# Optimization experiments

Measured on AMD Instinct MI355X. Metric: run time of the kernel, lower is better.

Reference implementation:

```python
import math
import jax, jax.numpy as jnp
import numpy as np

B, N, D, H = 8, 128, 256, 8
DK = D // H
SCALE = 0.02


def setup_inputs() -> dict:
    key = jax.random.key(0)
    ks = jax.random.split(key, 10)
    return {
        "query_node": jax.random.normal(ks[0], (B, N, D), jnp.float32),
        "value_node": jax.random.normal(ks[1], (B, N, D), jnp.float32),
        "key_edge": jax.random.normal(ks[2], (B, N, N, D), jnp.float32),
        "adj_matrix": jax.random.uniform(ks[3], (B, N, N), jnp.float32),  # pairwise distances >= 0
        "mask": jnp.ones((B, N), jnp.int32),
        "Wq": jax.random.normal(ks[4], (D, D), jnp.float32) * SCALE,
        "bq": jnp.zeros((D,), jnp.float32),
        "Wk": jax.random.normal(ks[5], (D, D), jnp.float32) * SCALE,
        "bk": jnp.zeros((D,), jnp.float32),
        "Wv": jax.random.normal(ks[6], (D, D), jnp.float32) * SCALE,
        "bv": jnp.zeros((D,), jnp.float32),
        "Wno": jax.random.normal(ks[7], (D, D), jnp.float32) * SCALE,
        "bno": jnp.zeros((D,), jnp.float32),
        "Weo": jax.random.normal(ks[8], (D, D), jnp.float32) * SCALE,
        "beo": jnp.zeros((D,), jnp.float32),
        "att_lambda": jnp.float32(0.1),
    }


def reference(query_node, value_node, key_edge, adj_matrix, mask,
              Wq, bq, Wk, bk, Wv, bv, Wno, bno, Weo, beo, att_lambda):
    # distance-kernelized adjacency: softmax(-lambda * dist) over neighbors
    adj = att_lambda * adj_matrix                                  # [B,N,N]
    adj = jnp.where(mask[:, None, :] == 0, jnp.inf, adj)
    adj = jax.nn.softmax(-adj, axis=-1)                            # [B,N,N]

    q = (query_node @ Wq.T + bq).reshape(B, N, H, DK).transpose(0, 2, 1, 3)      # [B,H,N,DK] bhmd
    k = (key_edge @ Wk.T + bk).reshape(B, N, N, H, DK).transpose(0, 3, 1, 2, 4)  # [B,H,N,N,DK] bhmnd
    v = (value_node @ Wv.T + bv).reshape(B, N, H, DK).transpose(0, 2, 1, 3)      # [B,H,N,DK] bhnd

    inv_sqrt = 1.0 / math.sqrt(DK)
    out_scores = jnp.einsum('bhmd,bhmnd->bhmn', q, k) * inv_sqrt
    in_scores = jnp.einsum('bhnd,bhmnd->bhnm', q, k) * inv_sqrt

    m4 = mask[:, None, None, :] == 0                               # [B,1,1,N]
    neg_inf = jnp.asarray(-jnp.inf, out_scores.dtype)
    out_scores = jnp.where(m4, neg_inf, out_scores)
    in_scores = jnp.where(m4, neg_inf, in_scores)

    out_attn = jax.nn.softmax(out_scores, axis=-1)
    in_attn = jax.nn.softmax(in_scores, axis=-1)

    # message = out_attn + in_attn - diag_embed(diag(out_attn))
    eye = jnp.eye(N, dtype=out_attn.dtype)
    message = out_attn + in_attn - out_attn * eye
    message = message * adj[:, None]                               # adjacency gating (dropout = identity at eval)

    node_hidden = jnp.einsum('bhmn,bhnd->bhmd', message, v)        # [B,H,N,DK]
    edge_hidden = message[..., None] * k                           # [B,H,N,N,DK] outer-product edge update

    node_hidden = node_hidden.transpose(0, 2, 1, 3).reshape(B, N, D)
    edge_hidden = edge_hidden.transpose(0, 2, 3, 1, 4).reshape(B, N, N, D)

    return (node_hidden @ Wno.T + bno, edge_hidden @ Weo.T + beo)
```

## Files before the change

kernel.cpp:

```cpp
#include <hip/hip_runtime.h>
#include <math.h>

#define Bc 8
#define Nc 128
#define Dc 256
#define Hc 8
#define DKc 32

typedef __attribute__((ext_vector_type(8))) short short8;
typedef __attribute__((ext_vector_type(4))) float floatx4;

__device__ __forceinline__ unsigned short f2bf(float f) {
  unsigned int u = __float_as_uint(f);
  u += 0x7FFFu + ((u >> 16) & 1u);
  return (unsigned short)(u >> 16);
}

__device__ __forceinline__ float bf2f(unsigned short s) {
  return __uint_as_float(((unsigned int)s) << 16);
}

__global__ __launch_bounds__(256) void cast_bf16_kernel(
    const float* __restrict__ src, unsigned short* __restrict__ dst, int n) {
  const int i = (blockIdx.x * 256 + threadIdx.x) * 4;
  if (i < n) {
    const float4 v = *(const float4*)&src[i];
    *(ushort4*)&dst[i] = make_ushort4(f2bf(v.x), f2bf(v.y), f2bf(v.z), f2bf(v.w));
  }
}

__global__ __launch_bounds__(256) void gemm_xwT_kernel(
    const float* __restrict__ X, const float* __restrict__ W,
    const float* __restrict__ bias, float* __restrict__ C, int M) {
  __shared__ float As[64][17];
  __shared__ float Ws[64][17];
  const int t = threadIdx.x;
  const int tx = t & 15;
  const int ty = t >> 4;
  const size_t row0 = (size_t)blockIdx.y * 64;
  const int col0 = blockIdx.x * 64;
  const int lr = t >> 2;
  const int lc = (t & 3) * 4;

  float acc[4][4] = {};

  for (int kk = 0; kk < 256; kk += 16) {
    float4 av = *(const float4*)&X[(row0 + lr) * 256 + kk + lc];
    float4 wv = *(const float4*)&W[(size_t)(col0 + lr) * 256 + kk + lc];
    As[lr][lc] = av.x; As[lr][lc + 1] = av.y; As[lr][lc + 2] = av.z; As[lr][lc + 3] = av.w;
    Ws[lr][lc] = wv.x; Ws[lr][lc + 1] = wv.y; Ws[lr][lc + 2] = wv.z; Ws[lr][lc + 3] = wv.w;
    __syncthreads();
#pragma unroll
    for (int e = 0; e < 16; ++e) {
      float a[4], w[4];
#pragma unroll
      for (int r = 0; r < 4; ++r) a[r] = As[ty * 4 + r][e];
#pragma unroll
      for (int c = 0; c < 4; ++c) w[c] = Ws[tx * 4 + c][e];
#pragma unroll
      for (int r = 0; r < 4; ++r)
#pragma unroll
        for (int c = 0; c < 4; ++c) acc[r][c] = fmaf(a[r], w[c], acc[r][c]);
    }
    __syncthreads();
  }

  const float4 bv = *(const float4*)&bias[col0 + tx * 4];
#pragma unroll
  for (int r = 0; r < 4; ++r) {
    float4 o;
    o.x = acc[r][0] + bv.x;
    o.y = acc[r][1] + bv.y;
    o.z = acc[r][2] + bv.z;
    o.w = acc[r][3] + bv.w;
    *(float4*)&C[(row0 + ty * 4 + r) * 256 + col0 + tx * 4] = o;
  }
}

__global__ __launch_bounds__(128) void adj_softmax_kernel(
    const float* __restrict__ adj, const int* __restrict__ mask,
    const float* __restrict__ lam_p, float* __restrict__ adjs) {
  __shared__ float red[128];
  const int bi = blockIdx.x;
  const int b = bi >> 7;
  const int j = threadIdx.x;
  const float lam = lam_p[0];
  float x = (mask[b * 128 + j] != 0) ? (-lam * adj[(size_t)bi * 128 + j]) : -INFINITY;
  red[j] = x; __syncthreads();
  for (int s = 64; s > 0; s >>= 1) { if (j < s) red[j] = fmaxf(red[j], red[j + s]); __syncthreads(); }
  const float mx = red[0]; __syncthreads();
  const float e = expf(x - mx);
  red[j] = e; __syncthreads();
  for (int s = 64; s > 0; s >>= 1) { if (j < s) red[j] += red[j + s]; __syncthreads(); }
  const float z = red[0];
  adjs[(size_t)bi * 128 + j] = e / z;
}

__global__ __launch_bounds__(256) void kscore_kernel(
    const float* __restrict__ ke, const float* __restrict__ q,
    const unsigned short* __restrict__ wk, const float* __restrict__ bk,
    float* __restrict__ osc, float* __restrict__ isc,
    float* __restrict__ edge ) {
  __shared__ __align__(16) unsigned short As[64 * 40];
  __shared__ __align__(16) unsigned short Ws[256 * 40];
  const int nblk = blockIdx.x;
  const int bm = blockIdx.y;
  const int b = bm >> 7;
  const int m = bm & 127;
  const int n0 = nblk * 64;
  const int t = threadIdx.x;
  const int l = t & 63;
  const int w = t >> 6;
  const int lr = l & 15;
  const int lk = l >> 4;
  const size_t rowbase = ((size_t)bm * 128 + n0) * 256;
  unsigned short* kbf = (unsigned short*)edge;

  floatx4 acc[4][4] = {};

  for (int kk = 0; kk < 256; kk += 32) {
    float4 av[2]; int arow[2], akc[2];
#pragma unroll
    for (int p = 0; p < 2; ++p) {
      const int f = p * 256 + t;
      arow[p] = f >> 3; akc[p] = (f & 7) * 4;
      av[p] = *(const float4*)&ke[rowbase + (size_t)arow[p] * 256 + kk + akc[p]];
    }
    uint4 wv[4];
#pragma unroll
    for (int p = 0; p < 4; ++p) {
      const int f = p * 256 + t;
      const int row = f >> 2, kc = (f & 3) * 8;
      wv[p] = *(const uint4*)&wk[(size_t)row * 256 + kk + kc];
    }
    __syncthreads();
#pragma unroll
    for (int p = 0; p < 2; ++p)
      *(ushort4*)&As[arow[p] * 40 + akc[p]] =
          make_ushort4(f2bf(av[p].x), f2bf(av[p].y), f2bf(av[p].z), f2bf(av[p].w));
#pragma unroll
    for (int p = 0; p < 4; ++p) {
      const int f = p * 256 + t;
      const int row = f >> 2, kc = (f & 3) * 8;
      *(uint4*)&Ws[row * 40 + kc] = wv[p];
    }
    __syncthreads();
    short8 a[4], bw[4];
#pragma unroll
    for (int i = 0; i < 4; ++i)
      a[i] = *(const short8*)&As[(i * 16 + lr) * 40 + lk * 8];
#pragma unroll
    for (int j = 0; j < 4; ++j)
      bw[j] = *(const short8*)&Ws[(w * 64 + j * 16 + lr) * 40 + lk * 8];
#pragma unroll
    for (int i = 0; i < 4; ++i)
#pragma unroll
      for (int j = 0; j < 4; ++j)
        acc[i][j] = __builtin_amdgcn_mfma_f32_16x16x32_bf16(bw[j], a[i], acc[i][j], 0, 0, 0);
  }

  const float inv_sqrt = 0.17677669529663687f;
  float4 qm4[4], kb4[4];
#pragma unroll
  for (int j = 0; j < 4; ++j) {
    qm4[j] = *(const float4*)&q[((size_t)(b * 128 + m)) * 256 + w * 64 + j * 16 + lk * 4];
    kb4[j] = *(const float4*)&bk[w * 64 + j * 16 + lk * 4];
  }
#pragma unroll
  for (int i = 0; i < 4; ++i) {
    const int ng = n0 + i * 16 + lr;
    const size_t gkb = (size_t)bm * 128 + ng;
    const size_t qnb = ((size_t)(b * 128 + ng)) * 256 + w * 64 + lk * 4;
    float po0 = 0.f, po1 = 0.f, pi0 = 0.f, pi1 = 0.f;
#pragma unroll
    for (int j = 0; j < 4; ++j) {
      const float4 qn = *(const float4*)&q[qnb + j * 16];
      const float k0 = acc[i][j][0] + kb4[j].x;
      const float k1 = acc[i][j][1] + kb4[j].y;
      const float k2 = acc[i][j][2] + kb4[j].z;
      const float k3 = acc[i][j][3] + kb4[j].w;
      *(ushort4*)&kbf[gkb * 512 + 256 + w * 64 + j * 16 + lk * 4] =
          make_ushort4(f2bf(k0), f2bf(k1), f2bf(k2), f2bf(k3));
      const float so = fmaf(k0, qm4[j].x, fmaf(k1, qm4[j].y, fmaf(k2, qm4[j].z, k3 * qm4[j].w)));
      const float si = fmaf(k0, qn.x, fmaf(k1, qn.y, fmaf(k2, qn.z, k3 * qn.w)));
      if (j < 2) { po0 += so; pi0 += si; } else { po1 += so; pi1 += si; }
    }
    po0 += __shfl_xor(po0, 16, 64); po0 += __shfl_xor(po0, 32, 64);
    po1 += __shfl_xor(po1, 16, 64); po1 += __shfl_xor(po1, 32, 64);
    pi0 += __shfl_xor(pi0, 16, 64); pi0 += __shfl_xor(pi0, 32, 64);
    pi1 += __shfl_xor(pi1, 16, 64); pi1 += __shfl_xor(pi1, 32, 64);
    if (lk == 0) {
      const int h0 = w * 2, h1 = w * 2 + 1;
      osc[((size_t)(b * 8 + h0) * 128 + m) * 128 + ng] = po0 * inv_sqrt;
      osc[((size_t)(b * 8 + h1) * 128 + m) * 128 + ng] = po1 * inv_sqrt;
      isc[((size_t)(b * 8 + h0) * 128 + ng) * 128 + m] = pi0 * inv_sqrt;
      isc[((size_t)(b * 8 + h1) * 128 + ng) * 128 + m] = pi1 * inv_sqrt;
    }
  }
}

__global__ __launch_bounds__(128) void message_kernel(
    const float* __restrict__ osc, const float* __restrict__ isc,
    const float* __restrict__ adjs, const int* __restrict__ mask,
    float* __restrict__ msg) {
  __shared__ float red[128];
  const int bhi = blockIdx.x;
  const int i = bhi & 127;
  const int b = bhi >> 10;
  const int j = threadIdx.x;
  const bool mj = mask[b * 128 + j] != 0;

  const float so = mj ? osc[(size_t)bhi * 128 + j] : -INFINITY;
  const float si = mj ? isc[(size_t)bhi * 128 + j] : -INFINITY;

  red[j] = so; __syncthreads();
  for (int s = 64; s > 0; s >>= 1) { if (j < s) red[j] = fmaxf(red[j], red[j + s]); __syncthreads(); }
  const float mo = red[0]; __syncthreads();
  const float eo = expf(so - mo);
  red[j] = eo; __syncthreads();
  for (int s = 64; s > 0; s >>= 1) { if (j < s) red[j] += red[j + s]; __syncthreads(); }
  const float zo = red[0]; __syncthreads();
  const float oa = eo / zo;

  red[j] = si; __syncthreads();
  for (int s = 64; s > 0; s >>= 1) { if (j < s) red[j] = fmaxf(red[j], red[j + s]); __syncthreads(); }
  const float mi = red[0]; __syncthreads();
  const float ei = expf(si - mi);
  red[j] = ei; __syncthreads();
  for (int s = 64; s > 0; s >>= 1) { if (j < s) red[j] += red[j + s]; __syncthreads(); }
  const float zi = red[0];
  const float ia = ei / zi;

  float val = oa + ia - ((i == j) ? oa : 0.0f);
  val *= adjs[((size_t)(b * 128 + i)) * 128 + j];
  msg[(size_t)bhi * 128 + j] = val;
}

__global__ __launch_bounds__(256) void node_hidden_kernel(
    const float* __restrict__ msg, const float* __restrict__ v,
    float* __restrict__ nh) {
  __shared__ float Ms[32][129];
  __shared__ float Vs[128][33];
  const int blk = blockIdx.x;
  const int mblk = blk & 3;
  const int bh = blk >> 2;
  const int h = bh & 7;
  const int b = bh >> 3;
  const int t = threadIdx.x;

  {
    const int n = t & 127, r0 = t >> 7;
#pragma unroll
    for (int p = 0; p < 16; ++p) {
      const int r = r0 + p * 2;
      Ms[r][n] = msg[((size_t)bh * 128 + mblk * 32 + r) * 128 + n];
    }
  }
  {
    const int dk = t & 31, n0 = t >> 5;
#pragma unroll
    for (int p = 0; p < 16; ++p) {
      const int n = n0 + p * 8;
      Vs[n][dk] = v[((size_t)b * 128 + n) * 256 + h * 32 + dk];
    }
  }
  __syncthreads();

  const int dk = t & 31;
  const int mg = t >> 5;
  float acc[4] = {0.f, 0.f, 0.f, 0.f};
  for (int n = 0; n < 128; ++n) {
    const float vv = Vs[n][dk];
#pragma unroll
    for (int r = 0; r < 4; ++r) acc[r] = fmaf(Ms[mg + 8 * r][n], vv, acc[r]);
  }
#pragma unroll
  for (int r = 0; r < 4; ++r) {
    const int m = mblk * 32 + mg + 8 * r;
    nh[((size_t)b * 128 + m) * 256 + h * 32 + dk] = acc[r];
  }
}

__global__ __launch_bounds__(256) void edge2_kernel(
    float* edge, const float* __restrict__ msg,
    const unsigned short* __restrict__ weo, const float* __restrict__ beo) {
  __shared__ __align__(16) unsigned short As[64 * 40];
  __shared__ __align__(16) unsigned short Ws[256 * 40];
  __shared__ float Msgs[64][8];
  const int nblk = blockIdx.x;
  const int bm = blockIdx.y;
  const int b = bm >> 7;
  const int m = bm & 127;
  const int n0 = nblk * 64;
  const int t = threadIdx.x;
  const int l = t & 63;
  const int w = t >> 6;
  const int lr = l & 15;
  const int lk = l >> 4;
  const unsigned short* kbf = (const unsigned short*)edge;
  const size_t g0 = (size_t)bm * 128 + n0;

#pragma unroll
  for (int p = 0; p < 2; ++p) {
    const int idx = t + p * 256;
    const int r = idx >> 3, h = idx & 7;
    Msgs[r][h] = msg[(((size_t)(b * 8 + h) * 128 + m) * 128) + n0 + r];
  }

  floatx4 acc[4][4] = {};
  const int arow = t >> 2, akc = (t & 3) * 8;

  for (int kk = 0; kk < 256; kk += 32) {
    const int h = kk >> 5;
    const uint4 kv = *(const uint4*)&kbf[(g0 + arow) * 512 + 256 + kk + akc];
    uint4 wv[4];
#pragma unroll
    for (int p = 0; p < 4; ++p) {
      const int f = p * 256 + t;
      const int row = f >> 2, kc = (f & 3) * 8;
      wv[p] = *(const uint4*)&weo[(size_t)row * 256 + kk + kc];
    }
    __syncthreads();
    {
      const float sc = Msgs[arow][h];
      const unsigned short* us = (const unsigned short*)&kv;
      unsigned short o[8];
#pragma unroll
      for (int e = 0; e < 8; ++e) o[e] = f2bf(bf2f(us[e]) * sc);
      *(ushort4*)&As[arow * 40 + akc]     = make_ushort4(o[0], o[1], o[2], o[3]);
      *(ushort4*)&As[arow * 40 + akc + 4] = make_ushort4(o[4], o[5], o[6], o[7]);
    }
#pragma unroll
    for (int p = 0; p < 4; ++p) {
      const int f = p * 256 + t;
      const int row = f >> 2, kc = (f & 3) * 8;
      *(uint4*)&Ws[row * 40 + kc] = wv[p];
    }
    __syncthreads();
    short8 a[4], bw[4];
#pragma unroll
    for (int i = 0; i < 4; ++i)
      a[i] = *(const short8*)&As[(i * 16 + lr) * 40 + lk * 8];
#pragma unroll
    for (int j = 0; j < 4; ++j)
      bw[j] = *(const short8*)&Ws[(w * 64 + j * 16 + lr) * 40 + lk * 8];
#pragma unroll
    for (int i = 0; i < 4; ++i)
#pragma unroll
      for (int j = 0; j < 4; ++j)
        acc[i][j] = __builtin_amdgcn_mfma_f32_16x16x32_bf16(bw[j], a[i], acc[i][j], 0, 0, 0);
  }

  float4 bj[4];
#pragma unroll
  for (int j = 0; j < 4; ++j) bj[j] = *(const float4*)&beo[w * 64 + j * 16 + lk * 4];
  const size_t rowbase = g0 * 256;
#pragma unroll
  for (int i = 0; i < 4; ++i) {
    const size_t rb = rowbase + (size_t)(i * 16 + lr) * 256;
#pragma unroll
    for (int j = 0; j < 4; ++j) {
      float4 o;
      o.x = acc[i][j][0] + bj[j].x;
      o.y = acc[i][j][1] + bj[j].y;
      o.z = acc[i][j][2] + bj[j].z;
      o.w = acc[i][j][3] + bj[j].w;
      *(float4*)&edge[rb + w * 64 + j * 16 + lk * 4] = o;
    }
  }
}

extern "C" void kernel_launch(void* const* d_in, const int* in_sizes, int n_in,
                              void* d_out, int out_size, void* d_ws, size_t ws_size,
                              hipStream_t stream) {
  (void)in_sizes; (void)n_in; (void)out_size; (void)ws_size;
  const float* query_node = (const float*)d_in[0];
  const float* value_node = (const float*)d_in[1];
  const float* key_edge   = (const float*)d_in[2];
  const float* adj_matrix = (const float*)d_in[3];
  const int*   mask       = (const int*)d_in[4];
  const float* Wq  = (const float*)d_in[5];
  const float* bq  = (const float*)d_in[6];
  const float* Wk  = (const float*)d_in[7];
  const float* bk  = (const float*)d_in[8];
  const float* Wv  = (const float*)d_in[9];
  const float* bv  = (const float*)d_in[10];
  const float* Wno = (const float*)d_in[11];
  const float* bno = (const float*)d_in[12];
  const float* Weo = (const float*)d_in[13];
  const float* beo = (const float*)d_in[14];
  const float* lam = (const float*)d_in[15];

  float* out = (float*)d_out;
  float* node_out = out;
  float* edge_out = out + (size_t)Bc * Nc * Dc;

  float* ws = (float*)d_ws;
  float* q    = ws; ws += (size_t)Bc * Nc * Dc;
  float* v    = ws; ws += (size_t)Bc * Nc * Dc;
  float* adjs = ws; ws += (size_t)Bc * Nc * Nc;
  float* osc  = ws; ws += (size_t)Bc * Hc * Nc * Nc;
  float* isc  = ws; ws += (size_t)Bc * Hc * Nc * Nc;
  float* msg  = ws; ws += (size_t)Bc * Hc * Nc * Nc;
  float* nh   = ws; ws += (size_t)Bc * Nc * Dc;
  unsigned short* wkbf  = (unsigned short*)ws; ws += 32768;
  unsigned short* weobf = (unsigned short*)ws; ws += 32768;

  cast_bf16_kernel<<<dim3(64), 256, 0, stream>>>(Wk, wkbf, Dc * Dc);
  cast_bf16_kernel<<<dim3(64), 256, 0, stream>>>(Weo, weobf, Dc * Dc);
  gemm_xwT_kernel<<<dim3(4, 16), 256, 0, stream>>>(query_node, Wq, bq, q, Bc * Nc);
  gemm_xwT_kernel<<<dim3(4, 16), 256, 0, stream>>>(value_node, Wv, bv, v, Bc * Nc);
  adj_softmax_kernel<<<dim3(Bc * Nc), 128, 0, stream>>>(adj_matrix, mask, lam, adjs);
  kscore_kernel<<<dim3(2, 1024), 256, 0, stream>>>(key_edge, q, wkbf, bk, osc, isc, edge_out);
  message_kernel<<<dim3(Bc * Hc * Nc), 128, 0, stream>>>(osc, isc, adjs, mask, msg);
  node_hidden_kernel<<<dim3(Bc * Hc * 4), 256, 0, stream>>>(msg, v, nh);
  gemm_xwT_kernel<<<dim3(4, 16), 256, 0, stream>>>(nh, Wno, bno, node_out, Bc * Nc);
  edge2_kernel<<<dim3(2, 1024), 256, 0, stream>>>(edge_out, msg, weobf, beo);
}
```

Measured before the change: 543.2 us.

## Load MFMA operands directly from global memory and transpose in-score layout

Both the key projection/score kernel and the edge output GEMM now drop their shared-memory staging tiles and barriers. Each lane loads its MFMA A and B fragments straight from global memory, converting to bf16 in registers. The in-direction scores are now written in the same coalesced layout as the out-scores, and the message kernel reads them with a strided gather instead. This removes LDS traffic and synchronisation but duplicates global and L2 reads of the weights across waves and moves uncoalesced access from the score writes to the message reads.

```diff
diff --git a/kernel.cpp b/kernel.cpp
--- a/kernel.cpp
+++ b/kernel.cpp
@@ -18,6 +18,15 @@
 
 __device__ __forceinline__ float bf2f(unsigned short s) {
   return __uint_as_float(((unsigned int)s) << 16);
+}
+
+__device__ __forceinline__ short8 f2bf8(float4 lo, float4 hi) {
+  short8 r;
+  r[0] = (short)f2bf(lo.x); r[1] = (short)f2bf(lo.y);
+  r[2] = (short)f2bf(lo.z); r[3] = (short)f2bf(lo.w);
+  r[4] = (short)f2bf(hi.x); r[5] = (short)f2bf(hi.y);
+  r[6] = (short)f2bf(hi.z); r[7] = (short)f2bf(hi.w);
+  return r;
 }
 
 __global__ __launch_bounds__(256) void cast_bf16_kernel(
@@ -99,10 +108,8 @@
 __global__ __launch_bounds__(256) void kscore_kernel(
     const float* __restrict__ ke, const float* __restrict__ q,
     const unsigned short* __restrict__ wk, const float* __restrict__ bk,
-    float* __restrict__ osc, float* __restrict__ isc,
+    float* __restrict__ osc, float* __restrict__ iscT,
     float* __restrict__ edge ) {
-  __shared__ __align__(16) unsigned short As[64 * 40];
-  __shared__ __align__(16) unsigned short Ws[256 * 40];
   const int nblk = blockIdx.x;
   const int bm = blockIdx.y;
   const int b = bm >> 7;
@@ -118,40 +125,20 @@
 
   floatx4 acc[4][4] = {};
 
-  for (int kk = 0; kk < 256; kk += 32) {
-    float4 av[2]; int arow[2], akc[2];
-#pragma unroll
-    for (int p = 0; p < 2; ++p) {
-      const int f = p * 256 + t;
-      arow[p] = f >> 3; akc[p] = (f & 7) * 4;
-      av[p] = *(const float4*)&ke[rowbase + (size_t)arow[p] * 256 + kk + akc[p]];
-    }
-    uint4 wv[4];
-#pragma unroll
-    for (int p = 0; p < 4; ++p) {
-      const int f = p * 256 + t;
-      const int row = f >> 2, kc = (f & 3) * 8;
-      wv[p] = *(const uint4*)&wk[(size_t)row * 256 + kk + kc];
-    }
-    __syncthreads();
-#pragma unroll
-    for (int p = 0; p < 2; ++p)
-      *(ushort4*)&As[arow[p] * 40 + akc[p]] =
-          make_ushort4(f2bf(av[p].x), f2bf(av[p].y), f2bf(av[p].z), f2bf(av[p].w));
-#pragma unroll
-    for (int p = 0; p < 4; ++p) {
-      const int f = p * 256 + t;
-      const int row = f >> 2, kc = (f & 3) * 8;
-      *(uint4*)&Ws[row * 40 + kc] = wv[p];
-    }
-    __syncthreads();
+#pragma unroll 2
+  for (int c = 0; c < 8; ++c) {
+    const int kk = c * 32;
     short8 a[4], bw[4];
 #pragma unroll
-    for (int i = 0; i < 4; ++i)
-      a[i] = *(const short8*)&As[(i * 16 + lr) * 40 + lk * 8];
+    for (int i = 0; i < 4; ++i) {
+      const size_t base = rowbase + (size_t)(i * 16 + lr) * 256 + kk + lk * 8;
+      const float4 f0 = *(const float4*)&ke[base];
+      const float4 f1 = *(const float4*)&ke[base + 4];
+      a[i] = f2bf8(f0, f1);
+    }
 #pragma unroll
     for (int j = 0; j < 4; ++j)
-      bw[j] = *(const short8*)&Ws[(w * 64 + j * 16 + lr) * 40 + lk * 8];
+      bw[j] = *(const short8*)&wk[(size_t)(w * 64 + j * 16 + lr) * 256 + kk + lk * 8];
 #pragma unroll
     for (int i = 0; i < 4; ++i)
 #pragma unroll
@@ -191,27 +178,28 @@
     pi1 += __shfl_xor(pi1, 16, 64); pi1 += __shfl_xor(pi1, 32, 64);
     if (lk == 0) {
       const int h0 = w * 2, h1 = w * 2 + 1;
-      osc[((size_t)(b * 8 + h0) * 128 + m) * 128 + ng] = po0 * inv_sqrt;
-      osc[((size_t)(b * 8 + h1) * 128 + m) * 128 + ng] = po1 * inv_sqrt;
-      isc[((size_t)(b * 8 + h0) * 128 + ng) * 128 + m] = pi0 * inv_sqrt;
-      isc[((size_t)(b * 8 + h1) * 128 + ng) * 128 + m] = pi1 * inv_sqrt;
+      osc [((size_t)(b * 8 + h0) * 128 + m) * 128 + ng] = po0 * inv_sqrt;
+      osc [((size_t)(b * 8 + h1) * 128 + m) * 128 + ng] = po1 * inv_sqrt;
+      iscT[((size_t)(b * 8 + h0) * 128 + m) * 128 + ng] = pi0 * inv_sqrt;
+      iscT[((size_t)(b * 8 + h1) * 128 + m) * 128 + ng] = pi1 * inv_sqrt;
     }
   }
 }
 
 __global__ __launch_bounds__(128) void message_kernel(
-    const float* __restrict__ osc, const float* __restrict__ isc,
+    const float* __restrict__ osc, const float* __restrict__ iscT,
     const float* __restrict__ adjs, const int* __restrict__ mask,
     float* __restrict__ msg) {
   __shared__ float red[128];
   const int bhi = blockIdx.x;
   const int i = bhi & 127;
+  const int bh = bhi >> 7;
   const int b = bhi >> 10;
   const int j = threadIdx.x;
   const bool mj = mask[b * 128 + j] != 0;
 
   const float so = mj ? osc[(size_t)bhi * 128 + j] : -INFINITY;
-  const float si = mj ? isc[(size_t)bhi * 128 + j] : -INFINITY;
+  const float si = mj ? iscT[((size_t)bh * 128 + j) * 128 + i] : -INFINITY;
 
   red[j] = so; __syncthreads();
   for (int s = 64; s > 0; s >>= 1) { if (j < s) red[j] = fmaxf(red[j], red[j + s]); __syncthreads(); }
@@ -284,9 +272,6 @@
 __global__ __launch_bounds__(256) void edge2_kernel(
     float* edge, const float* __restrict__ msg,
     const unsigned short* __restrict__ weo, const float* __restrict__ beo) {
-  __shared__ __align__(16) unsigned short As[64 * 40];
-  __shared__ __align__(16) unsigned short Ws[256 * 40];
-  __shared__ float Msgs[64][8];
   const int nblk = blockIdx.x;
   const int bm = blockIdx.y;
   const int b = bm >> 7;
@@ -300,56 +285,32 @@
   const unsigned short* kbf = (const unsigned short*)edge;
   const size_t g0 = (size_t)bm * 128 + n0;
 
-#pragma unroll
-  for (int p = 0; p < 2; ++p) {
-    const int idx = t + p * 256;
-    const int r = idx >> 3, h = idx & 7;
-    Msgs[r][h] = msg[(((size_t)(b * 8 + h) * 128 + m) * 128) + n0 + r];
-  }
-
   floatx4 acc[4][4] = {};
-  const int arow = t >> 2, akc = (t & 3) * 8;
-
-  for (int kk = 0; kk < 256; kk += 32) {
-    const int h = kk >> 5;
-    const uint4 kv = *(const uint4*)&kbf[(g0 + arow) * 512 + 256 + kk + akc];
-    uint4 wv[4];
-#pragma unroll
-    for (int p = 0; p < 4; ++p) {
-      const int f = p * 256 + t;
-      const int row = f >> 2, kc = (f & 3) * 8;
-      wv[p] = *(const uint4*)&weo[(size_t)row * 256 + kk + kc];
-    }
-    __syncthreads();
-    {
-      const float sc = Msgs[arow][h];
-      const unsigned short* us = (const unsigned short*)&kv;
-      unsigned short o[8];
-#pragma unroll
-      for (int e = 0; e < 8; ++e) o[e] = f2bf(bf2f(us[e]) * sc);
-      *(ushort4*)&As[arow * 40 + akc]     = make_ushort4(o[0], o[1], o[2], o[3]);
-      *(ushort4*)&As[arow * 40 + akc + 4] = make_ushort4(o[4], o[5], o[6], o[7]);
-    }
-#pragma unroll
-    for (int p = 0; p < 4; ++p) {
-      const int f = p * 256 + t;
-      const int row = f >> 2, kc = (f & 3) * 8;
-      *(uint4*)&Ws[row * 40 + kc] = wv[p];
-    }
-    __syncthreads();
+
+#pragma unroll 2
+  for (int c = 0; c < 8; ++c) {
+    const int kk = c * 32;
     short8 a[4], bw[4];
 #pragma unroll
-    for (int i = 0; i < 4; ++i)
-      a[i] = *(const short8*)&As[(i * 16 + lr) * 40 + lk * 8];
+    for (int i = 0; i < 4; ++i) {
+      const int row = i * 16 + lr;
+      const short8 kv = *(const short8*)&kbf[(g0 + row) * 512 + 256 + kk + lk * 8];
+      const float sc = msg[(((size_t)(b * 8 + c) * 128 + m)) * 128 + n0 + row];
+#pragma unroll
+      for (int e = 0; e < 8; ++e)
+        a[i][e] = (short)f2bf(bf2f((unsigned short)kv[e]) * sc);
+    }
 #pragma unroll
     for (int j = 0; j < 4; ++j)
-      bw[j] = *(const short8*)&Ws[(w * 64 + j * 16 + lr) * 40 + lk * 8];
+      bw[j] = *(const short8*)&weo[(size_t)(w * 64 + j * 16 + lr) * 256 + kk + lk * 8];
 #pragma unroll
     for (int i = 0; i < 4; ++i)
 #pragma unroll
       for (int j = 0; j < 4; ++j)
         acc[i][j] = __builtin_amdgcn_mfma_f32_16x16x32_bf16(bw[j], a[i], acc[i][j], 0, 0, 0);
   }
+
+  __syncthreads();
 
   float4 bj[4];
 #pragma unroll
@@ -400,7 +361,7 @@
   float* v    = ws; ws += (size_t)Bc * Nc * Dc;
   float* adjs = ws; ws += (size_t)Bc * Nc * Nc;
   float* osc  = ws; ws += (size_t)Bc * Hc * Nc * Nc;
-  float* isc  = ws; ws += (size_t)Bc * Hc * Nc * Nc;
+  float* iscT = ws; ws += (size_t)Bc * Hc * Nc * Nc;
   float* msg  = ws; ws += (size_t)Bc * Hc * Nc * Nc;
   float* nh   = ws; ws += (size_t)Bc * Nc * Dc;
   unsigned short* wkbf  = (unsigned short*)ws; ws += 32768;
@@ -411,8 +372,8 @@
   gemm_xwT_kernel<<<dim3(4, 16), 256, 0, stream>>>(query_node, Wq, bq, q, Bc * Nc);
   gemm_xwT_kernel<<<dim3(4, 16), 256, 0, stream>>>(value_node, Wv, bv, v, Bc * Nc);
   adj_softmax_kernel<<<dim3(Bc * Nc), 128, 0, stream>>>(adj_matrix, mask, lam, adjs);
-  kscore_kernel<<<dim3(2, 1024), 256, 0, stream>>>(key_edge, q, wkbf, bk, osc, isc, edge_out);
-  message_kernel<<<dim3(Bc * Hc * Nc), 128, 0, stream>>>(osc, isc, adjs, mask, msg);
+  kscore_kernel<<<dim3(2, 1024), 256, 0, stream>>>(key_edge, q, wkbf, bk, osc, iscT, edge_out);
+  message_kernel<<<dim3(Bc * Hc * Nc), 128, 0, stream>>>(osc, iscT, adjs, mask, msg);
   node_hidden_kernel<<<dim3(Bc * Hc * 4), 256, 0, stream>>>(msg, v, nh);
   gemm_xwT_kernel<<<dim3(4, 16), 256, 0, stream>>>(nh, Wno, bno, node_out, Bc * Nc);
   edge2_kernel<<<dim3(2, 1024), 256, 0, stream>>>(edge_out, msg, weobf, beo);
```

New measurement: 489.5 us. -9.9%, faster.
